# Kernel tuning notes

Hardware: AMD Instinct MI355X
Metric: run time of the kernel (lower is better)

Reference implementation:

```python
import jax, jax.numpy as jnp
import numpy as np

USR_NUM = 100000
D_IN = 32
D_HID = 32
D_MID = 16
D_OUT = 2
N_EDGES = 1600000
EPS = 1e-16  # matches torch_geometric.utils.softmax denominator eps


def _glorot(key, shape):
    fan_in, fan_out = shape[0], shape[1]
    lim = np.sqrt(6.0 / (fan_in + fan_out))
    return jax.random.uniform(key, shape, jnp.float32, -lim, lim)


def setup_inputs() -> dict:
    key = jax.random.key(0)
    ks = jax.random.split(key, 16)
    inp = {
        "edge_index": jax.random.randint(ks[0], (2, N_EDGES), 0, USR_NUM, dtype=jnp.int64)
        if jax.config.jax_enable_x64 else jax.random.randint(ks[0], (2, N_EDGES), 0, USR_NUM).astype(jnp.int32),
        "emb": jax.random.normal(ks[1], (USR_NUM, D_IN), jnp.float32),
        # conv1: TransformerConv(32 -> 32, heads=1)
        "Wq1": _glorot(ks[2], (D_IN, D_HID)), "bq1": jnp.zeros((D_HID,), jnp.float32),
        "Wk1": _glorot(ks[3], (D_IN, D_HID)), "bk1": jnp.zeros((D_HID,), jnp.float32),
        "Wv1": _glorot(ks[4], (D_IN, D_HID)), "bv1": jnp.zeros((D_HID,), jnp.float32),
        "Ws1": _glorot(ks[5], (D_IN, D_HID)), "bs1": jnp.zeros((D_HID,), jnp.float32),
        # conv2: TransformerConv(32 -> 16, heads=1)
        "Wq2": _glorot(ks[6], (D_HID, D_MID)), "bq2": jnp.zeros((D_MID,), jnp.float32),
        "Wk2": _glorot(ks[7], (D_HID, D_MID)), "bk2": jnp.zeros((D_MID,), jnp.float32),
        "Wv2": _glorot(ks[8], (D_HID, D_MID)), "bv2": jnp.zeros((D_MID,), jnp.float32),
        "Ws2": _glorot(ks[9], (D_HID, D_MID)), "bs2": jnp.zeros((D_MID,), jnp.float32),
        # output: Linear(16 -> 2)
        "Wo": _glorot(ks[10], (D_MID, D_OUT)), "bo": jnp.zeros((D_OUT,), jnp.float32),
    }
    return inp


def transformer_conv(x, src, dst, Wq, bq, Wk, bk, Wv, bv, Ws, bs, n_nodes):
    # edge (j=src -> i=dst): alpha_ij = softmax_i( <q_i, k_j> / sqrt(d) )
    d = Wq.shape[1]
    q = (x @ Wq + bq)[dst]          # [E, d]
    k = (x @ Wk + bk)[src]          # [E, d]
    v = (x @ Wv + bv)[src]          # [E, d]
    alpha = jnp.sum(q * k, axis=-1) / jnp.sqrt(jnp.float32(d))  # [E]
    # segment softmax over incoming edges of each destination node
    seg_max = jax.ops.segment_max(alpha, dst, num_segments=n_nodes)  # [N]
    e = jnp.exp(alpha - seg_max[dst])
    seg_sum = jax.ops.segment_sum(e, dst, num_segments=n_nodes)      # [N]
    w = e / (seg_sum[dst] + EPS)
    agg = jax.ops.segment_sum(v * w[:, None], dst, num_segments=n_nodes)  # [N, d]
    return agg + x @ Ws + bs  # root/skip connection (PyG default root_weight=True)


def reference(edge_index, emb,
              Wq1, bq1, Wk1, bk1, Wv1, bv1, Ws1, bs1,
              Wq2, bq2, Wk2, bk2, Wv2, bv2, Ws2, bs2,
              Wo, bo):
    src, dst = edge_index[0], edge_index[1]
    h = transformer_conv(emb, src, dst, Wq1, bq1, Wk1, bk1, Wv1, bv1, Ws1, bs1, USR_NUM)
    h = jax.nn.relu(h)
    h = transformer_conv(h, src, dst, Wq2, bq2, Wk2, bk2, Wv2, bv2, Ws2, bs2, USR_NUM)
    h = jax.nn.relu(h)
    return h @ Wo + bo  # [N, 2]
```

## Files before the change

### kernel.cpp

```cpp
#include <hip/hip_runtime.h>
#include <hip/hip_bf16.h>

typedef __hip_bfloat16 bf16;
typedef unsigned int uint;
typedef unsigned short ushort;

#define N_NODES 100000
#define N_EDGES_C 1600000
#define NSB 196
#define NSBP 200
#define SBCAP 10240
#define RND 2048
#define EPB (RND / 256)
#define NBIN 64
#define CNT_N (NBIN * NSB)

__device__ __forceinline__ float ldf(const void* p, long i, int isbf) {
    return isbf ? __bfloat162float(((const bf16*)p)[i]) : ((const float*)p)[i];
}
__device__ __forceinline__ int ldidx(const int* ei, long pos, int is64) {
    return is64 ? ei[2 * pos] : ei[pos];
}
__device__ __forceinline__ ushort bfb(float x) {
    bf16 h = __float2bfloat16(x);
    return *(ushort*)&h;
}
__device__ __forceinline__ float bl(uint u) { return __uint_as_float(u << 16); }
__device__ __forceinline__ float bh(uint u) { return __uint_as_float(u & 0xFFFF0000u); }

__global__ void setup_kernel(
    const void* emb, const int* ei,
    const void* Wq1, const void* bq1, const void* Wk1, const void* bk1,
    const void* Wv1, const void* bv1, const void* Ws1, const void* bs1,
    const void* Wq2, const void* bq2, const void* Wk2, const void* bk2,
    const void* Wv2, const void* bv2, const void* Ws2, const void* bs2,
    const void* Wo, const void* bo,
    int* flags, float* wp1, float* bp1, float* wp2, float* bp2, float* woF,
    int* curSB) {
    __shared__ int sf0;
    int t = threadIdx.x;
    if (t == 0) {
        const bf16* pb = (const bf16*)emb;
        int big = 0;
        for (int i = 0; i < 256; i++) {
            float v = __bfloat162float(pb[i]);
            if (!(v > -1.0e6f && v < 1.0e6f)) big++;
        }
        int f0 = (big <= 8) ? 1 : 0;
        int nz = 0;
        for (int i = 1; i < 256; i += 2) nz += (ei[i] != 0) ? 1 : 0;
        flags[0] = f0;
        flags[1] = (nz == 0) ? 1 : 0;
        sf0 = f0;
    }
    __syncthreads();
    int isbf = sf0;
    for (int i = t; i < 1024; i += 256) {
        wp1[i]        = ldf(Wq1, i, isbf);
        wp1[1024 + i] = ldf(Wk1, i, isbf);
        wp1[2048 + i] = ldf(Wv1, i, isbf);
        wp1[3072 + i] = ldf(Ws1, i, isbf);
    }
    for (int i = t; i < 512; i += 256) {
        wp2[i]        = ldf(Wq2, i, isbf);
        wp2[512 + i]  = ldf(Wk2, i, isbf);
        wp2[1024 + i] = ldf(Wv2, i, isbf);
        wp2[1536 + i] = ldf(Ws2, i, isbf);
    }
    if (t < 32) {
        bp1[t] = ldf(bq1, t, isbf); bp1[32 + t] = ldf(bk1, t, isbf);
        bp1[64 + t] = ldf(bv1, t, isbf); bp1[96 + t] = ldf(bs1, t, isbf);
        woF[t] = ldf(Wo, t, isbf);
    }
    if (t < 16) {
        bp2[t] = ldf(bq2, t, isbf); bp2[16 + t] = ldf(bk2, t, isbf);
        bp2[32 + t] = ldf(bv2, t, isbf); bp2[48 + t] = ldf(bs2, t, isbf);
    }
    if (t < 2) woF[32 + t] = ldf(bo, t, isbf);
    curSB[t] = 0;
}

__global__ void radix_a(const int* __restrict__ ei, const int* __restrict__ flags,
                        int* __restrict__ curSB, uint* __restrict__ pairsSB) {
    __shared__ int cnt[256];
    __shared__ int excl[256];
    __shared__ int gbase[NSBP];
    __shared__ uint sVal[RND];
    __shared__ unsigned char sSb[RND];
    const int is64 = flags[1];
    int t = threadIdx.x;
    cnt[t] = 0;
    __syncthreads();
    long base = (long)blockIdx.x * RND;

    int mySb[EPB]; int myRank[EPB]; uint myPk[EPB];
#pragma unroll
    for (int r = 0; r < EPB; r++) {
        long e = base + r * 256 + t;
        mySb[r] = -1;
        if (e < N_EDGES_C) {
            int d = ldidx(ei, (long)N_EDGES_C + e, is64);
            int s = ldidx(ei, e, is64);
            int sb = d >> 9;
            myPk[r] = (uint)s | ((uint)(d & 511) << 17);
            myRank[r] = atomicAdd(&cnt[sb], 1);
            mySb[r] = sb;
        }
    }
    __syncthreads();
    int v = cnt[t];
    excl[t] = v;
    __syncthreads();
    for (int off = 1; off < 256; off <<= 1) {
        int u = (t >= off) ? excl[t - off] : 0;
        __syncthreads();
        excl[t] += u;
        __syncthreads();
    }
    int myExcl = excl[t] - v;
    __syncthreads();
    excl[t] = myExcl;
    __syncthreads();
#pragma unroll
    for (int r = 0; r < EPB; r++) {
        if (mySb[r] >= 0) {
            int pos = excl[mySb[r]] + myRank[r];
            sVal[pos] = myPk[r];
            sSb[pos] = (unsigned char)mySb[r];
        }
    }
    __syncthreads();
    if (t < NSBP)
        gbase[t] = (cnt[t] > 0) ? atomicAdd(&curSB[t], cnt[t]) : 0;
    __syncthreads();
    int tot = excl[NSBP - 1] + cnt[NSBP - 1];
    for (int i = t; i < tot; i += 256) {
        int sb = sSb[i];
        int gp = gbase[sb] + (i - excl[sb]);
        if (gp < SBCAP)
            pairsSB[(size_t)sb * SBCAP + gp] = sVal[i];
    }
}

__global__ void radix_b(const int* __restrict__ curSB, const uint* __restrict__ pairsSB,
                        int* __restrict__ esrc,
                        int* __restrict__ rowbeg, int* __restrict__ rowend,
                        int* __restrict__ cntBins) {
    __shared__ uint sP[SBCAP];
    __shared__ int dcnt[512], dexcl[512], dcur[512];
    __shared__ int hbin[NBIN];
    int sb = blockIdx.x;
    int t = threadIdx.x;
    int n = min(curSB[sb], SBCAP);
    dcnt[t] = 0; dcur[t] = 0;
    if (t < NBIN) hbin[t] = 0;
    __syncthreads();
    for (int i = t; i < n; i += 512) {
        uint pk = pairsSB[(size_t)sb * SBCAP + i];
        sP[i] = pk;
        atomicAdd(&dcnt[(pk >> 17) & 511], 1);
    }
    __syncthreads();
    int v = dcnt[t];
    dexcl[t] = v;
    __syncthreads();
    for (int off = 1; off < 512; off <<= 1) {
        int u = (t >= off) ? dexcl[t - off] : 0;
        __syncthreads();
        dexcl[t] += u;
        __syncthreads();
    }
    int myExcl = dexcl[t] - v;
    __syncthreads();
    dexcl[t] = myExcl;
    __syncthreads();
    const int EB = sb * SBCAP;
    int dst = sb * 512 + t;
    if (dst < N_NODES) {
        rowbeg[dst] = EB + dexcl[t];
        rowend[dst] = EB + dexcl[t] + dcnt[t];
        atomicAdd(&hbin[min(dcnt[t], NBIN - 1)], 1);
    }
    for (int i = t; i < n; i += 512) {
        uint pk = sP[i];
        int j = (pk >> 17) & 511;
        int p = dexcl[j] + atomicAdd(&dcur[j], 1);
        esrc[EB + p] = (int)(pk & 0x1FFFF);
    }
    __syncthreads();
    if (t < NBIN) cntBins[t * NSB + sb] = hbin[t];
}

__global__ void scan_all(int* __restrict__ x) {
    __shared__ int buf[CNT_N];
    __shared__ int part[1024];
    int t = threadIdx.x;
    for (int i = t; i < CNT_N; i += 1024) buf[i] = x[i];
    __syncthreads();
    const int C = (CNT_N + 1023) / 1024;
    int lo = t * C, hi = min(lo + C, CNT_N);
    int sum = 0;
    for (int i = lo; i < hi; i++) sum += buf[i];
    int v = sum;
    part[t] = v;
    __syncthreads();
    for (int off = 1; off < 1024; off <<= 1) {
        int u = (t >= off) ? part[t - off] : 0;
        __syncthreads();
        part[t] += u;
        __syncthreads();
    }
    int run = part[t] - v;
    for (int i = lo; i < hi; i++) { int val = buf[i]; buf[i] = run; run += val; }
    __syncthreads();
    for (int i = t; i < CNT_N; i += 1024) x[i] = buf[i];
}

__global__ void perm_scatter3(const int* __restrict__ rowbeg, const int* __restrict__ rowend,
                              int* __restrict__ basearr, int* __restrict__ perm) {
    __shared__ int cur[NBIN];
    int t = threadIdx.x, sb = blockIdx.x;
    if (t < NBIN) cur[t] = 0;
    __syncthreads();
    int i = sb * 512 + t;
    if (i < N_NODES) {
        int d = min(rowend[i] - rowbeg[i], NBIN - 1);
        int r = atomicAdd(&cur[d], 1);
        perm[basearr[d * NSB + sb] + r] = i;
    }
}

template <int DOUT, bool RUNTIME_DTYPE>
__global__ void node_linear(const void* __restrict__ X,
                            const float* __restrict__ wpack,
                            const float* __restrict__ bpack,
                            const int* __restrict__ flags,
                            float* __restrict__ q, ushort* __restrict__ kvb,
                            float* __restrict__ s) {
    const int TPN = DOUT / 4;
    const int NPB = 256 / TPN;
    const int W_ELEMS = 4 * 32 * DOUT;
    __shared__ float sW[W_ELEMS];
    __shared__ float sb[4 * DOUT];
    __shared__ float sX[NPB * 36];

    const float4* wp4 = (const float4*)wpack;
    float4* sW4 = (float4*)sW;
    for (int i = threadIdx.x; i < W_ELEMS / 4; i += 256) sW4[i] = wp4[i];
    if (threadIdx.x < 4 * DOUT) sb[threadIdx.x] = bpack[threadIdx.x];
    const int base = blockIdx.x * NPB * 32;
    bool useBf = RUNTIME_DTYPE && (flags[0] != 0);
    if (useBf) {
        for (int i = threadIdx.x; i < NPB * 32; i += 256) {
            int g = base + i;
            float xv = (g < N_NODES * 32) ? __bfloat162float(((const bf16*)X)[g]) : 0.0f;
            sX[(i >> 5) * 36 + (i & 31)] = xv;
        }
    } else {
        for (int i = threadIdx.x; i < NPB * 32; i += 256) {
            int g = base + i;
            sX[(i >> 5) * 36 + (i & 31)] = (g < N_NODES * 32) ? ((const float*)X)[g] : 0.0f;
        }
    }
    __syncthreads();

    int l = threadIdx.x / TPN;
    int c4 = (threadIdx.x % TPN) * 4;
    int n = blockIdx.x * NPB + l;
    if (n >= N_NODES) return;

    float xr[32];
#pragma unroll
    for (int j = 0; j < 8; j++) {
        float4 t = *(const float4*)&sX[l * 36 + 4 * j];
        xr[4 * j] = t.x; xr[4 * j + 1] = t.y; xr[4 * j + 2] = t.z; xr[4 * j + 3] = t.w;
    }
    float acc[4][4];
#pragma unroll
    for (int m = 0; m < 4; m++)
#pragma unroll
        for (int j = 0; j < 4; j++) acc[m][j] = sb[m * DOUT + c4 + j];

#pragma unroll
    for (int t = 0; t < 32; t++) {
#pragma unroll
        for (int m = 0; m < 4; m++) {
            float4 w = *(const float4*)&sW[(m * 32 + t) * DOUT + c4];
            acc[m][0] += xr[t] * w.x;
            acc[m][1] += xr[t] * w.y;
            acc[m][2] += xr[t] * w.z;
            acc[m][3] += xr[t] * w.w;
        }
    }
    size_t o = (size_t)n * DOUT + c4;
    *(float4*)&q[o] = make_float4(acc[0][0], acc[0][1], acc[0][2], acc[0][3]);
    *(float4*)&s[o] = make_float4(acc[3][0], acc[3][1], acc[3][2], acc[3][3]);
    size_t okv = (size_t)n * 2 * DOUT + c4;
    ushort4 kp = make_ushort4(bfb(acc[1][0]), bfb(acc[1][1]), bfb(acc[1][2]), bfb(acc[1][3]));
    ushort4 vp = make_ushort4(bfb(acc[2][0]), bfb(acc[2][1]), bfb(acc[2][2]), bfb(acc[2][3]));
    *(ushort4*)&kvb[okv]        = kp;
    *(ushort4*)&kvb[okv + DOUT] = vp;
}

template <int D, bool LAYER2>
__global__ void gather_attn(const int* __restrict__ perm,
                            const int* __restrict__ rowbeg, const int* __restrict__ rowend,
                            const int* __restrict__ esrc,
                            const float* __restrict__ q, const ushort* __restrict__ kvb,
                            const float* __restrict__ s,
                            const float* __restrict__ woF,
                            const int* __restrict__ flags,
                            float* __restrict__ h1o, void* __restrict__ out) {
    const int LPD = D / 8;
    const int G = 64 / LPD;
    int lane = threadIdx.x & 63;
    int wave = (blockIdx.x * blockDim.x + threadIdx.x) >> 6;
    int g = lane / LPD;
    int c = lane % LPD;
    int idx = wave * G + g;
    if (idx >= N_NODES) return;
    int dst = perm[(N_NODES - 1) - idx];

    const float rsq = (D == 32) ? 0.17677669529663689f : 0.25f;
    float4 qa = *(const float4*)(q + (size_t)dst * D + 8 * c);
    float4 qb = *(const float4*)(q + (size_t)dst * D + 8 * c + 4);
    int beg = rowbeg[dst], end = rowend[dst];

    const char* kvbase = (const char*)kvb;
    const int ROW = 4 * D;
    const int koff = 16 * c;
    const int voff = 2 * D + 16 * c;

    float sum0 = 0.f, sum1 = 0.f;
    float a0[8] = {0,0,0,0,0,0,0,0};
    float a1[8] = {0,0,0,0,0,0,0,0};

    uint4 kq[4], vq[4];
#pragma unroll
    for (int r = 0; r < 4; r++) {
        int sn = (beg + r < end) ? esrc[beg + r] : 0;
        const char* p = kvbase + (size_t)sn * ROW;
        kq[r] = *(const uint4*)(p + koff);
        vq[r] = *(const uint4*)(p + voff);
    }

    for (int e = beg; e < end; e += 4) {
        uint4 kc[4], vc[4];
#pragma unroll
        for (int r = 0; r < 4; r++) { kc[r] = kq[r]; vc[r] = vq[r]; }
#pragma unroll
        for (int r = 0; r < 4; r++) {
            if (e + 4 + r < end) {
                const char* p = kvbase + (size_t)esrc[e + 4 + r] * ROW;
                kq[r] = *(const uint4*)(p + koff);
                vq[r] = *(const uint4*)(p + voff);
            }
        }
#pragma unroll
        for (int r = 0; r < 4; r++) {
            if (e + r < end) {
                uint4 kA = kc[r], vA = vc[r];
                float pd = qa.x * bl(kA.x) + qa.y * bh(kA.x) + qa.z * bl(kA.y) + qa.w * bh(kA.y)
                         + qb.x * bl(kA.z) + qb.y * bh(kA.z) + qb.z * bl(kA.w) + qb.w * bh(kA.w);
#pragma unroll
                for (int m = LPD / 2; m >= 1; m >>= 1) pd += __shfl_xor(pd, m, LPD);
                float ex = __expf(fminf(fmaxf(pd * rsq, -80.0f), 80.0f));
                if (r & 1) {
                    sum1 += ex;
                    a1[0] += bl(vA.x) * ex; a1[1] += bh(vA.x) * ex;
                    a1[2] += bl(vA.y) * ex; a1[3] += bh(vA.y) * ex;
                    a1[4] += bl(vA.z) * ex; a1[5] += bh(vA.z) * ex;
                    a1[6] += bl(vA.w) * ex; a1[7] += bh(vA.w) * ex;
                } else {
                    sum0 += ex;
                    a0[0] += bl(vA.x) * ex; a0[1] += bh(vA.x) * ex;
                    a0[2] += bl(vA.y) * ex; a0[3] += bh(vA.y) * ex;
                    a0[4] += bl(vA.z) * ex; a0[5] += bh(vA.z) * ex;
                    a0[6] += bl(vA.w) * ex; a0[7] += bh(vA.w) * ex;
                }
            }
        }
    }
    float inv = 1.0f / (sum0 + sum1 + 1e-16f);
    float4 sa = *(const float4*)(s + (size_t)dst * D + 8 * c);
    float4 sb2 = *(const float4*)(s + (size_t)dst * D + 8 * c + 4);
    float h[8];
    h[0] = (a0[0] + a1[0]) * inv + sa.x;  h[1] = (a0[1] + a1[1]) * inv + sa.y;
    h[2] = (a0[2] + a1[2]) * inv + sa.z;  h[3] = (a0[3] + a1[3]) * inv + sa.w;
    h[4] = (a0[4] + a1[4]) * inv + sb2.x; h[5] = (a0[5] + a1[5]) * inv + sb2.y;
    h[6] = (a0[6] + a1[6]) * inv + sb2.z; h[7] = (a0[7] + a1[7]) * inv + sb2.w;
#pragma unroll
    for (int j = 0; j < 8; j++) h[j] = h[j] > 0.0f ? h[j] : 0.0f;

    if (!LAYER2) {
        *(float4*)(h1o + (size_t)dst * D + 8 * c)     = make_float4(h[0], h[1], h[2], h[3]);
        *(float4*)(h1o + (size_t)dst * D + 8 * c + 4) = make_float4(h[4], h[5], h[6], h[7]);
    } else {
        float p0 = 0.f, p1 = 0.f;
#pragma unroll
        for (int j = 0; j < 8; j++) {
            p0 += h[j] * woF[(8 * c + j) * 2 + 0];
            p1 += h[j] * woF[(8 * c + j) * 2 + 1];
        }
#pragma unroll
        for (int m = LPD / 2; m >= 1; m >>= 1) {
            p0 += __shfl_xor(p0, m, LPD);
            p1 += __shfl_xor(p1, m, LPD);
        }
        if (c == 0) {
            float o0 = p0 + woF[32];
            float o1 = p1 + woF[33];
            if (flags[0]) {
                ((bf16*)out)[dst * 2 + 0] = __float2bfloat16(o0);
                ((bf16*)out)[dst * 2 + 1] = __float2bfloat16(o1);
            } else {
                ((float*)out)[dst * 2 + 0] = o0;
                ((float*)out)[dst * 2 + 1] = o1;
            }
        }
    }
}

extern "C" void kernel_launch(void* const* d_in, const int* in_sizes, int n_in,
                              void* d_out, int out_size, void* d_ws, size_t ws_size,
                              hipStream_t stream) {
    const int* ei  = (const int*)d_in[0];
    const void* emb = d_in[1];
    const void *Wq1 = d_in[2],  *bq1 = d_in[3];
    const void *Wk1 = d_in[4],  *bk1 = d_in[5];
    const void *Wv1 = d_in[6],  *bv1 = d_in[7];
    const void *Ws1 = d_in[8],  *bs1 = d_in[9];
    const void *Wq2 = d_in[10], *bq2 = d_in[11];
    const void *Wk2 = d_in[12], *bk2 = d_in[13];
    const void *Wv2 = d_in[14], *bv2 = d_in[15];
    const void *Ws2 = d_in[16], *bs2 = d_in[17];
    const void *Wo  = d_in[18], *bo  = d_in[19];

    const size_t ND = (size_t)N_NODES * 32;
    const size_t SBTOT = (size_t)NSB * SBCAP;
    float* base   = (float*)d_ws;
    int*   flags  = (int*)base;
    float* wp1    = base + 64;
    float* bp1    = wp1 + 4096;
    float* wp2    = bp1 + 128;
    float* bp2    = wp2 + 2048;
    float* woF    = bp2 + 64;
    int*   curSB  = (int*)(woF + 64);
    int*   cnt    = curSB + 256;
    int*   rowbeg = cnt + 12800;
    int*   rowend = rowbeg + N_NODES;
    int*   perm   = rowend + N_NODES;
    float* uni    = (float*)(perm + N_NODES);
    uint*  pairsSB = (uint*)uni;
    float* q      = uni;
    float* s      = uni + ND;
    ushort* kvb   = (ushort*)(uni + 2 * ND);
    float* h1     = uni + 3 * ND;
    int*   esrc   = (int*)(uni + 4 * ND);

    const int B = 256;
    const int gNL32   = (N_NODES + 31) / 32;
    const int gNL16   = (N_NODES + 63) / 64;
    const int gGat32  = ((N_NODES + 15) / 16 * 64 + B - 1) / B;
    const int gGat16  = ((N_NODES + 31) / 32 * 64 + B - 1) / B;
    const int gRadA   = (N_EDGES_C + RND - 1) / RND;

    setup_kernel<<<1, B, 0, stream>>>(emb, ei,
        Wq1, bq1, Wk1, bk1, Wv1, bv1, Ws1, bs1,
        Wq2, bq2, Wk2, bk2, Wv2, bv2, Ws2, bs2, Wo, bo,
        flags, wp1, bp1, wp2, bp2, woF, curSB);

    radix_a<<<gRadA, B, 0, stream>>>(ei, flags, curSB, pairsSB);
    radix_b<<<NSB, 512, 0, stream>>>(curSB, pairsSB, esrc, rowbeg, rowend, cnt);

    scan_all<<<1, 1024, 0, stream>>>(cnt);
    perm_scatter3<<<NSB, 512, 0, stream>>>(rowbeg, rowend, cnt, perm);

    node_linear<32, true><<<gNL32, B, 0, stream>>>(emb, wp1, bp1, flags, q, kvb, s);
    gather_attn<32, false><<<gGat32, B, 0, stream>>>(
        perm, rowbeg, rowend, esrc, q, kvb, s, woF, flags, h1, nullptr);

    node_linear<16, false><<<gNL16, B, 0, stream>>>(h1, wp2, bp2, flags, q, kvb, s);
    gather_attn<16, true><<<gGat16, B, 0, stream>>>(
        perm, rowbeg, rowend, esrc, q, kvb, s, woF, flags, nullptr, d_out);
}
```

Measured before the change: 281.9 us.

## Fuse radix pass with layer-1 linear, drop global bin scan, fuse layer-2 projection into gather

Merges the first radix partition and the layer-1 node projection into one launch by splitting the grid, with shared memory in a union. The global degree-bin scan and perm scatter kernels are removed; each super-block now sorts its nodes by degree locally and writes a padded perm slot array with -1 sentinels. The layer-1 gather kernel now computes the layer-2 Q/K/V/skip projection in-block from shared memory, so the h1 intermediate and the separate layer-2 linear launch go away. This cuts four launches and a round trip through global memory. In exchange, degree balancing is now only local to each super-block, and the gather grids cover padded slots.

```diff
diff --git a/kernel.cpp b/kernel.cpp
--- a/kernel.cpp
+++ b/kernel.cpp
@@ -13,7 +13,8 @@
 #define RND 2048
 #define EPB (RND / 256)
 #define NBIN 64
-#define CNT_N (NBIN * NSB)
+#define G_RAD ((N_EDGES_C + RND - 1) / RND)
+#define NSLOT (NSB * 512)
 
 __device__ __forceinline__ float ldf(const void* p, long i, int isbf) {
     return isbf ? __bfloat162float(((const bf16*)p)[i]) : ((const float*)p)[i];
@@ -39,19 +40,26 @@
     int* curSB) {
     __shared__ int sf0;
     int t = threadIdx.x;
-    if (t == 0) {
+    if (t < 64) {
         const bf16* pb = (const bf16*)emb;
-        int big = 0;
-        for (int i = 0; i < 256; i++) {
+        int bad = 0;
+        for (int i = t; i < 256; i += 64) {
             float v = __bfloat162float(pb[i]);
-            if (!(v > -1.0e6f && v < 1.0e6f)) big++;
-        }
-        int f0 = (big <= 8) ? 1 : 0;
+            if (!(v > -1.0e6f && v < 1.0e6f)) bad++;
+        }
         int nz = 0;
-        for (int i = 1; i < 256; i += 2) nz += (ei[i] != 0) ? 1 : 0;
-        flags[0] = f0;
-        flags[1] = (nz == 0) ? 1 : 0;
-        sf0 = f0;
+        for (int i = 2 * t + 1; i < 256; i += 128) nz += (ei[i] != 0) ? 1 : 0;
+#pragma unroll
+        for (int m = 32; m >= 1; m >>= 1) {
+            bad += __shfl_xor(bad, m, 64);
+            nz  += __shfl_xor(nz, m, 64);
+        }
+        if (t == 0) {
+            int f0 = (bad <= 8) ? 1 : 0;
+            flags[0] = f0;
+            flags[1] = (nz == 0) ? 1 : 0;
+            sf0 = f0;
+        }
     }
     __syncthreads();
     int isbf = sf0;
@@ -80,175 +88,21 @@
     curSB[t] = 0;
 }
 
-__global__ void radix_a(const int* __restrict__ ei, const int* __restrict__ flags,
-                        int* __restrict__ curSB, uint* __restrict__ pairsSB) {
-    __shared__ int cnt[256];
-    __shared__ int excl[256];
-    __shared__ int gbase[NSBP];
-    __shared__ uint sVal[RND];
-    __shared__ unsigned char sSb[RND];
-    const int is64 = flags[1];
-    int t = threadIdx.x;
-    cnt[t] = 0;
-    __syncthreads();
-    long base = (long)blockIdx.x * RND;
-
-    int mySb[EPB]; int myRank[EPB]; uint myPk[EPB];
-#pragma unroll
-    for (int r = 0; r < EPB; r++) {
-        long e = base + r * 256 + t;
-        mySb[r] = -1;
-        if (e < N_EDGES_C) {
-            int d = ldidx(ei, (long)N_EDGES_C + e, is64);
-            int s = ldidx(ei, e, is64);
-            int sb = d >> 9;
-            myPk[r] = (uint)s | ((uint)(d & 511) << 17);
-            myRank[r] = atomicAdd(&cnt[sb], 1);
-            mySb[r] = sb;
-        }
-    }
-    __syncthreads();
-    int v = cnt[t];
-    excl[t] = v;
-    __syncthreads();
-    for (int off = 1; off < 256; off <<= 1) {
-        int u = (t >= off) ? excl[t - off] : 0;
-        __syncthreads();
-        excl[t] += u;
-        __syncthreads();
-    }
-    int myExcl = excl[t] - v;
-    __syncthreads();
-    excl[t] = myExcl;
-    __syncthreads();
-#pragma unroll
-    for (int r = 0; r < EPB; r++) {
-        if (mySb[r] >= 0) {
-            int pos = excl[mySb[r]] + myRank[r];
-            sVal[pos] = myPk[r];
-            sSb[pos] = (unsigned char)mySb[r];
-        }
-    }
-    __syncthreads();
-    if (t < NSBP)
-        gbase[t] = (cnt[t] > 0) ? atomicAdd(&curSB[t], cnt[t]) : 0;
-    __syncthreads();
-    int tot = excl[NSBP - 1] + cnt[NSBP - 1];
-    for (int i = t; i < tot; i += 256) {
-        int sb = sSb[i];
-        int gp = gbase[sb] + (i - excl[sb]);
-        if (gp < SBCAP)
-            pairsSB[(size_t)sb * SBCAP + gp] = sVal[i];
-    }
-}
-
-__global__ void radix_b(const int* __restrict__ curSB, const uint* __restrict__ pairsSB,
-                        int* __restrict__ esrc,
-                        int* __restrict__ rowbeg, int* __restrict__ rowend,
-                        int* __restrict__ cntBins) {
-    __shared__ uint sP[SBCAP];
-    __shared__ int dcnt[512], dexcl[512], dcur[512];
-    __shared__ int hbin[NBIN];
-    int sb = blockIdx.x;
-    int t = threadIdx.x;
-    int n = min(curSB[sb], SBCAP);
-    dcnt[t] = 0; dcur[t] = 0;
-    if (t < NBIN) hbin[t] = 0;
-    __syncthreads();
-    for (int i = t; i < n; i += 512) {
-        uint pk = pairsSB[(size_t)sb * SBCAP + i];
-        sP[i] = pk;
-        atomicAdd(&dcnt[(pk >> 17) & 511], 1);
-    }
-    __syncthreads();
-    int v = dcnt[t];
-    dexcl[t] = v;
-    __syncthreads();
-    for (int off = 1; off < 512; off <<= 1) {
-        int u = (t >= off) ? dexcl[t - off] : 0;
-        __syncthreads();
-        dexcl[t] += u;
-        __syncthreads();
-    }
-    int myExcl = dexcl[t] - v;
-    __syncthreads();
-    dexcl[t] = myExcl;
-    __syncthreads();
-    const int EB = sb * SBCAP;
-    int dst = sb * 512 + t;
-    if (dst < N_NODES) {
-        rowbeg[dst] = EB + dexcl[t];
-        rowend[dst] = EB + dexcl[t] + dcnt[t];
-        atomicAdd(&hbin[min(dcnt[t], NBIN - 1)], 1);
-    }
-    for (int i = t; i < n; i += 512) {
-        uint pk = sP[i];
-        int j = (pk >> 17) & 511;
-        int p = dexcl[j] + atomicAdd(&dcur[j], 1);
-        esrc[EB + p] = (int)(pk & 0x1FFFF);
-    }
-    __syncthreads();
-    if (t < NBIN) cntBins[t * NSB + sb] = hbin[t];
-}
-
-__global__ void scan_all(int* __restrict__ x) {
-    __shared__ int buf[CNT_N];
-    __shared__ int part[1024];
-    int t = threadIdx.x;
-    for (int i = t; i < CNT_N; i += 1024) buf[i] = x[i];
-    __syncthreads();
-    const int C = (CNT_N + 1023) / 1024;
-    int lo = t * C, hi = min(lo + C, CNT_N);
-    int sum = 0;
-    for (int i = lo; i < hi; i++) sum += buf[i];
-    int v = sum;
-    part[t] = v;
-    __syncthreads();
-    for (int off = 1; off < 1024; off <<= 1) {
-        int u = (t >= off) ? part[t - off] : 0;
-        __syncthreads();
-        part[t] += u;
-        __syncthreads();
-    }
-    int run = part[t] - v;
-    for (int i = lo; i < hi; i++) { int val = buf[i]; buf[i] = run; run += val; }
-    __syncthreads();
-    for (int i = t; i < CNT_N; i += 1024) x[i] = buf[i];
-}
-
-__global__ void perm_scatter3(const int* __restrict__ rowbeg, const int* __restrict__ rowend,
-                              int* __restrict__ basearr, int* __restrict__ perm) {
-    __shared__ int cur[NBIN];
-    int t = threadIdx.x, sb = blockIdx.x;
-    if (t < NBIN) cur[t] = 0;
-    __syncthreads();
-    int i = sb * 512 + t;
-    if (i < N_NODES) {
-        int d = min(rowend[i] - rowbeg[i], NBIN - 1);
-        int r = atomicAdd(&cur[d], 1);
-        perm[basearr[d * NSB + sb] + r] = i;
-    }
-}
-
 template <int DOUT, bool RUNTIME_DTYPE>
-__global__ void node_linear(const void* __restrict__ X,
-                            const float* __restrict__ wpack,
-                            const float* __restrict__ bpack,
-                            const int* __restrict__ flags,
-                            float* __restrict__ q, ushort* __restrict__ kvb,
-                            float* __restrict__ s) {
+__device__ __forceinline__ void node_linear_body(
+    const void* __restrict__ X, const float* __restrict__ wpack,
+    const float* __restrict__ bpack, const int* __restrict__ flags,
+    float* __restrict__ q, ushort* __restrict__ kvb, float* __restrict__ s,
+    int bid, float* __restrict__ sW, float* __restrict__ sbias, float* __restrict__ sX) {
     const int TPN = DOUT / 4;
     const int NPB = 256 / TPN;
     const int W_ELEMS = 4 * 32 * DOUT;
-    __shared__ float sW[W_ELEMS];
-    __shared__ float sb[4 * DOUT];
-    __shared__ float sX[NPB * 36];
 
     const float4* wp4 = (const float4*)wpack;
     float4* sW4 = (float4*)sW;
     for (int i = threadIdx.x; i < W_ELEMS / 4; i += 256) sW4[i] = wp4[i];
-    if (threadIdx.x < 4 * DOUT) sb[threadIdx.x] = bpack[threadIdx.x];
-    const int base = blockIdx.x * NPB * 32;
+    if (threadIdx.x < 4 * DOUT) sbias[threadIdx.x] = bpack[threadIdx.x];
+    const int base = bid * NPB * 32;
     bool useBf = RUNTIME_DTYPE && (flags[0] != 0);
     if (useBf) {
         for (int i = threadIdx.x; i < NPB * 32; i += 256) {
@@ -266,20 +120,20 @@
 
     int l = threadIdx.x / TPN;
     int c4 = (threadIdx.x % TPN) * 4;
-    int n = blockIdx.x * NPB + l;
+    int n = bid * NPB + l;
     if (n >= N_NODES) return;
 
     float xr[32];
 #pragma unroll
     for (int j = 0; j < 8; j++) {
-        float4 t = *(const float4*)&sX[l * 36 + 4 * j];
-        xr[4 * j] = t.x; xr[4 * j + 1] = t.y; xr[4 * j + 2] = t.z; xr[4 * j + 3] = t.w;
+        float4 t4 = *(const float4*)&sX[l * 36 + 4 * j];
+        xr[4 * j] = t4.x; xr[4 * j + 1] = t4.y; xr[4 * j + 2] = t4.z; xr[4 * j + 3] = t4.w;
     }
     float acc[4][4];
 #pragma unroll
     for (int m = 0; m < 4; m++)
 #pragma unroll
-        for (int j = 0; j < 4; j++) acc[m][j] = sb[m * DOUT + c4 + j];
+        for (int j = 0; j < 4; j++) acc[m][j] = sbias[m * DOUT + c4 + j];
 
 #pragma unroll
     for (int t = 0; t < 32; t++) {
@@ -302,29 +156,195 @@
     *(ushort4*)&kvb[okv + DOUT] = vp;
 }
 
+struct RadixS {
+    int cnt[256]; int excl[256]; int gbase[NSBP];
+    uint sVal[RND]; unsigned char sSb[RND];
+};
+struct LinS { float sW[4096]; float sbias[128]; float sX[32 * 36]; };
+union alignas(16) FusedS { RadixS r; LinS l; };
+
+__global__ void fused_ra_nl(
+    const int* __restrict__ ei, const int* __restrict__ flags,
+    int* __restrict__ curSB, uint* __restrict__ pairsSB,
+    const void* __restrict__ X, const float* __restrict__ wpack,
+    const float* __restrict__ bpack,
+    float* __restrict__ q, ushort* __restrict__ kvb, float* __restrict__ s) {
+    __shared__ FusedS u;
+    if (blockIdx.x >= G_RAD) {
+        node_linear_body<32, true>(X, wpack, bpack, flags, q, kvb, s,
+                                   (int)blockIdx.x - G_RAD, u.l.sW, u.l.sbias, u.l.sX);
+        return;
+    }
+    int* cnt = u.r.cnt; int* excl = u.r.excl; int* gbase = u.r.gbase;
+    uint* sVal = u.r.sVal; unsigned char* sSb = u.r.sSb;
+    const int is64 = flags[1];
+    int t = threadIdx.x;
+    cnt[t] = 0;
+    __syncthreads();
+    long base = (long)blockIdx.x * RND;
+
+    int mySb[EPB]; int myRank[EPB]; uint myPk[EPB];
+#pragma unroll
+    for (int r = 0; r < EPB; r++) {
+        long e = base + r * 256 + t;
+        mySb[r] = -1;
+        if (e < N_EDGES_C) {
+            int d = ldidx(ei, (long)N_EDGES_C + e, is64);
+            int src = ldidx(ei, e, is64);
+            int sb = d >> 9;
+            myPk[r] = (uint)src | ((uint)(d & 511) << 17);
+            myRank[r] = atomicAdd(&cnt[sb], 1);
+            mySb[r] = sb;
+        }
+    }
+    __syncthreads();
+    int v = cnt[t];
+    excl[t] = v;
+    __syncthreads();
+    for (int off = 1; off < 256; off <<= 1) {
+        int u2 = (t >= off) ? excl[t - off] : 0;
+        __syncthreads();
+        excl[t] += u2;
+        __syncthreads();
+    }
+    int myExcl = excl[t] - v;
+    __syncthreads();
+    excl[t] = myExcl;
+    __syncthreads();
+#pragma unroll
+    for (int r = 0; r < EPB; r++) {
+        if (mySb[r] >= 0) {
+            int pos = excl[mySb[r]] + myRank[r];
+            sVal[pos] = myPk[r];
+            sSb[pos] = (unsigned char)mySb[r];
+        }
+    }
+    __syncthreads();
+    if (t < NSBP)
+        gbase[t] = (cnt[t] > 0) ? atomicAdd(&curSB[t], cnt[t]) : 0;
+    __syncthreads();
+    int tot = excl[NSBP - 1] + cnt[NSBP - 1];
+    for (int i = t; i < tot; i += 256) {
+        int sb = sSb[i];
+        int gp = gbase[sb] + (i - excl[sb]);
+        if (gp < SBCAP)
+            pairsSB[(size_t)sb * SBCAP + gp] = sVal[i];
+    }
+}
+
+__global__ void radix_b(const int* __restrict__ curSB, const uint* __restrict__ pairsSB,
+                        int* __restrict__ esrc,
+                        int* __restrict__ rowbeg, int* __restrict__ rowend,
+                        int* __restrict__ perm) {
+    __shared__ uint sP[SBCAP];
+    __shared__ int dcnt[512], dexcl[512], dcur[512];
+    __shared__ int hbin[NBIN], hbase[NBIN], hcur[NBIN];
+    int sb = blockIdx.x;
+    int t = threadIdx.x;
+    int n = min(curSB[sb], SBCAP);
+    dcnt[t] = 0; dcur[t] = 0;
+    if (t < NBIN) { hbin[t] = 0; hcur[t] = 0; }
+    perm[sb * 512 + t] = -1;
+    __syncthreads();
+    for (int i = t; i < n; i += 512) {
+        uint pk = pairsSB[(size_t)sb * SBCAP + i];
+        sP[i] = pk;
+        atomicAdd(&dcnt[(pk >> 17) & 511], 1);
+    }
+    __syncthreads();
+    int v = dcnt[t];
+    dexcl[t] = v;
+    __syncthreads();
+    for (int off = 1; off < 512; off <<= 1) {
+        int u2 = (t >= off) ? dexcl[t - off] : 0;
+        __syncthreads();
+        dexcl[t] += u2;
+        __syncthreads();
+    }
+    int myExcl = dexcl[t] - v;
+    __syncthreads();
+    dexcl[t] = myExcl;
+    __syncthreads();
+    const int EB = sb * SBCAP;
+    int dst = sb * 512 + t;
+    int mybin = -1;
+    if (dst < N_NODES) {
+        rowbeg[dst] = EB + myExcl;
+        rowend[dst] = EB + myExcl + v;
+        mybin = min(v, NBIN - 1);
+        atomicAdd(&hbin[mybin], 1);
+    }
+    __syncthreads();
+    if (t < 64) {
+        int hv = hbin[t];
+        int sfx = hv;
+#pragma unroll
+        for (int off = 1; off < 64; off <<= 1) {
+            int u2 = __shfl_down(sfx, off, 64);
+            if (t + off < 64) sfx += u2;
+        }
+        hbase[t] = sfx - hv;
+    }
+    __syncthreads();
+    if (dst < N_NODES) {
+        int r = atomicAdd(&hcur[mybin], 1);
+        perm[sb * 512 + hbase[mybin] + r] = dst;
+    }
+    for (int i = t; i < n; i += 512) {
+        uint pk = sP[i];
+        int j = (pk >> 17) & 511;
+        int p2 = dexcl[j] + atomicAdd(&dcur[j], 1);
+        esrc[EB + p2] = (int)(pk & 0x1FFFF);
+    }
+}
+
 template <int D, bool LAYER2>
 __global__ void gather_attn(const int* __restrict__ perm,
                             const int* __restrict__ rowbeg, const int* __restrict__ rowend,
                             const int* __restrict__ esrc,
                             const float* __restrict__ q, const ushort* __restrict__ kvb,
                             const float* __restrict__ s,
+                            const float* __restrict__ wp2,
+                            const float* __restrict__ bp2,
                             const float* __restrict__ woF,
                             const int* __restrict__ flags,
-                            float* __restrict__ h1o, void* __restrict__ out) {
+                            float* __restrict__ q2o, ushort* __restrict__ kvb2o,
+                            float* __restrict__ s2o,
+                            void* __restrict__ out) {
     const int LPD = D / 8;
     const int G = 64 / LPD;
+    __shared__ float sW2[2048];
+    __shared__ float sb2[64];
+    __shared__ float sH[64 * 36];
+    __shared__ int sDst[64];
+
+    if constexpr (!LAYER2) {
+        for (int i = threadIdx.x; i < 2048; i += 256) sW2[i] = wp2[i];
+        if (threadIdx.x < 64) sb2[threadIdx.x] = bp2[threadIdx.x];
+    }
+
     int lane = threadIdx.x & 63;
     int wave = (blockIdx.x * blockDim.x + threadIdx.x) >> 6;
     int g = lane / LPD;
     int c = lane % LPD;
     int idx = wave * G + g;
-    if (idx >= N_NODES) return;
-    int dst = perm[(N_NODES - 1) - idx];
+    if constexpr (LAYER2) {
+        if (idx >= NSLOT) return;
+    }
+    int dst = perm[idx];
+    if constexpr (LAYER2) {
+        if (dst < 0) return;
+    }
+    bool alive = (dst >= 0);
 
     const float rsq = (D == 32) ? 0.17677669529663689f : 0.25f;
-    float4 qa = *(const float4*)(q + (size_t)dst * D + 8 * c);
-    float4 qb = *(const float4*)(q + (size_t)dst * D + 8 * c + 4);
-    int beg = rowbeg[dst], end = rowend[dst];
+    float4 qa = make_float4(0.f, 0.f, 0.f, 0.f), qb = qa;
+    int beg = 0, end = 0;
+    if (alive) {
+        qa = *(const float4*)(q + (size_t)dst * D + 8 * c);
+        qb = *(const float4*)(q + (size_t)dst * D + 8 * c + 4);
+        beg = rowbeg[dst]; end = rowend[dst];
+    }
 
     const char* kvbase = (const char*)kvb;
     const int ROW = 4 * D;
@@ -382,19 +402,57 @@
         }
     }
     float inv = 1.0f / (sum0 + sum1 + 1e-16f);
-    float4 sa = *(const float4*)(s + (size_t)dst * D + 8 * c);
-    float4 sb2 = *(const float4*)(s + (size_t)dst * D + 8 * c + 4);
+    float4 sa = make_float4(0.f, 0.f, 0.f, 0.f), sbv = sa;
+    if (alive) {
+        sa  = *(const float4*)(s + (size_t)dst * D + 8 * c);
+        sbv = *(const float4*)(s + (size_t)dst * D + 8 * c + 4);
+    }
     float h[8];
     h[0] = (a0[0] + a1[0]) * inv + sa.x;  h[1] = (a0[1] + a1[1]) * inv + sa.y;
     h[2] = (a0[2] + a1[2]) * inv + sa.z;  h[3] = (a0[3] + a1[3]) * inv + sa.w;
-    h[4] = (a0[4] + a1[4]) * inv + sb2.x; h[5] = (a0[5] + a1[5]) * inv + sb2.y;
-    h[6] = (a0[6] + a1[6]) * inv + sb2.z; h[7] = (a0[7] + a1[7]) * inv + sb2.w;
+    h[4] = (a0[4] + a1[4]) * inv + sbv.x; h[5] = (a0[5] + a1[5]) * inv + sbv.y;
+    h[6] = (a0[6] + a1[6]) * inv + sbv.z; h[7] = (a0[7] + a1[7]) * inv + sbv.w;
 #pragma unroll
     for (int j = 0; j < 8; j++) h[j] = h[j] > 0.0f ? h[j] : 0.0f;
 
-    if (!LAYER2) {
-        *(float4*)(h1o + (size_t)dst * D + 8 * c)     = make_float4(h[0], h[1], h[2], h[3]);
-        *(float4*)(h1o + (size_t)dst * D + 8 * c + 4) = make_float4(h[4], h[5], h[6], h[7]);
+    if constexpr (!LAYER2) {
+        int gl = (threadIdx.x >> 6) * G + g;
+        if (alive) {
+            *(float4*)&sH[gl * 36 + 8 * c]     = make_float4(h[0], h[1], h[2], h[3]);
+            *(float4*)&sH[gl * 36 + 8 * c + 4] = make_float4(h[4], h[5], h[6], h[7]);
+        }
+        if (c == 0) sDst[gl] = dst;
+        __syncthreads();
+        int l = threadIdx.x >> 2;
+        int c4 = (threadIdx.x & 3) * 4;
+        int nd = sDst[l];
+        if (nd >= 0) {
+            float acc2[4][4];
+#pragma unroll
+            for (int m = 0; m < 4; m++)
+#pragma unroll
+                for (int j = 0; j < 4; j++) acc2[m][j] = sb2[m * 16 + c4 + j];
+#pragma unroll
+            for (int t2 = 0; t2 < 32; t2++) {
+                float xv = sH[l * 36 + t2];
+#pragma unroll
+                for (int m = 0; m < 4; m++) {
+                    float4 w = *(const float4*)&sW2[(m * 32 + t2) * 16 + c4];
+                    acc2[m][0] += xv * w.x;
+                    acc2[m][1] += xv * w.y;
+                    acc2[m][2] += xv * w.z;
+                    acc2[m][3] += xv * w.w;
+                }
+            }
+            size_t o = (size_t)nd * 16 + c4;
+            *(float4*)&q2o[o] = make_float4(acc2[0][0], acc2[0][1], acc2[0][2], acc2[0][3]);
+            *(float4*)&s2o[o] = make_float4(acc2[3][0], acc2[3][1], acc2[3][2], acc2[3][3]);
+            size_t okv = (size_t)nd * 32 + c4;
+            ushort4 kp = make_ushort4(bfb(acc2[1][0]), bfb(acc2[1][1]), bfb(acc2[1][2]), bfb(acc2[1][3]));
+            ushort4 vp = make_ushort4(bfb(acc2[2][0]), bfb(acc2[2][1]), bfb(acc2[2][2]), bfb(acc2[2][3]));
+            *(ushort4*)&kvb2o[okv]      = kp;
+            *(ushort4*)&kvb2o[okv + 16] = vp;
+        }
     } else {
         float p0 = 0.f, p1 = 0.f;
 #pragma unroll
@@ -436,7 +494,8 @@
     const void *Ws2 = d_in[16], *bs2 = d_in[17];
     const void *Wo  = d_in[18], *bo  = d_in[19];
 
-    const size_t ND = (size_t)N_NODES * 32;
+    const size_t ND   = (size_t)N_NODES * 32;
+    const size_t ND16 = (size_t)N_NODES * 16;
     const size_t SBTOT = (size_t)NSB * SBCAP;
     float* base   = (float*)d_ws;
     int*   flags  = (int*)base;
@@ -446,41 +505,40 @@
     float* bp2    = wp2 + 2048;
     float* woF    = bp2 + 64;
     int*   curSB  = (int*)(woF + 64);
-    int*   cnt    = curSB + 256;
-    int*   rowbeg = cnt + 12800;
+    int*   rowbeg = curSB + 256;
     int*   rowend = rowbeg + N_NODES;
     int*   perm   = rowend + N_NODES;
-    float* uni    = (float*)(perm + N_NODES);
-    uint*  pairsSB = (uint*)uni;
-    float* q      = uni;
-    float* s      = uni + ND;
-    ushort* kvb   = (ushort*)(uni + 2 * ND);
-    float* h1     = uni + 3 * ND;
-    int*   esrc   = (int*)(uni + 4 * ND);
+    float* p      = (float*)(perm + NSLOT);
+    float* q      = p; p += ND;
+    float* s      = p; p += ND;
+    ushort* kvb   = (ushort*)p; p += ND;
+    float* q2     = p; p += ND16;
+    float* s2     = p; p += ND16;
+    ushort* kvb2  = (ushort*)p; p += ND16;
+    int*   esrc   = (int*)p; p += SBTOT;
+    uint*  pairsSB = (uint*)p;
 
     const int B = 256;
-    const int gNL32   = (N_NODES + 31) / 32;
-    const int gNL16   = (N_NODES + 63) / 64;
-    const int gGat32  = ((N_NODES + 15) / 16 * 64 + B - 1) / B;
-    const int gGat16  = ((N_NODES + 31) / 32 * 64 + B - 1) / B;
-    const int gRadA   = (N_EDGES_C + RND - 1) / RND;
+    const int gNL32  = (N_NODES + 31) / 32;
+    const int gFused = G_RAD + gNL32;
+    const int gG1    = NSLOT / 64;
+    const int gG2    = NSLOT / 128;
 
     setup_kernel<<<1, B, 0, stream>>>(emb, ei,
         Wq1, bq1, Wk1, bk1, Wv1, bv1, Ws1, bs1,
         Wq2, bq2, Wk2, bk2, Wv2, bv2, Ws2, bs2, Wo, bo,
         flags, wp1, bp1, wp2, bp2, woF, curSB);
 
-    radix_a<<<gRadA, B, 0, stream>>>(ei, flags, curSB, pairsSB);
-    radix_b<<<NSB, 512, 0, stream>>>(curSB, pairsSB, esrc, rowbeg, rowend, cnt);
-
-    scan_all<<<1, 1024, 0, stream>>>(cnt);
-    perm_scatter3<<<NSB, 512, 0, stream>>>(rowbeg, rowend, cnt, perm);
-
-    node_linear<32, true><<<gNL32, B, 0, stream>>>(emb, wp1, bp1, flags, q, kvb, s);
-    gather_attn<32, false><<<gGat32, B, 0, stream>>>(
-        perm, rowbeg, rowend, esrc, q, kvb, s, woF, flags, h1, nullptr);
-
-    node_linear<16, false><<<gNL16, B, 0, stream>>>(h1, wp2, bp2, flags, q, kvb, s);
-    gather_attn<16, true><<<gGat16, B, 0, stream>>>(
-        perm, rowbeg, rowend, esrc, q, kvb, s, woF, flags, nullptr, d_out);
-}
+    fused_ra_nl<<<gFused, B, 0, stream>>>(ei, flags, curSB, pairsSB,
+                                          emb, wp1, bp1, q, kvb, s);
+
+    radix_b<<<NSB, 512, 0, stream>>>(curSB, pairsSB, esrc, rowbeg, rowend, perm);
+
+    gather_attn<32, false><<<gG1, B, 0, stream>>>(
+        perm, rowbeg, rowend, esrc, q, kvb, s, wp2, bp2, nullptr, flags,
+        q2, kvb2, s2, nullptr);
+
+    gather_attn<16, true><<<gG2, B, 0, stream>>>(
+        perm, rowbeg, rowend, esrc, q2, kvb2, s2, nullptr, nullptr, woF, flags,
+        nullptr, nullptr, nullptr, d_out);
+}
```

Measured after the change: 265.8 us. 5.7% less time.
